# Kernel tuning notes

Hardware: AMD Instinct MI355X
Metric: run time of the kernel (lower is better)

## Reference

```python
import jax, jax.numpy as jnp
import numpy as np

DIM = 1024
HEADS = 16

def setup_inputs() -> dict:
    key = jax.random.key(0)
    ks = jax.random.split(key, 5)
    x = jax.random.normal(ks[0], (4, 2048, DIM), dtype=jnp.float32)
    s = 1.0 / np.sqrt(DIM)
    Wqkv = jax.random.normal(ks[1], (DIM, 3 * DIM), dtype=jnp.float32) * s
    bqkv = jnp.zeros((3 * DIM,), dtype=jnp.float32)
    Wproj = jax.random.normal(ks[2], (DIM, DIM), dtype=jnp.float32) * s
    bproj = jnp.zeros((DIM,), dtype=jnp.float32)
    return {"x": x, "Wqkv": Wqkv, "bqkv": bqkv, "Wproj": Wproj, "bproj": bproj}

def reference(x, Wqkv, bqkv, Wproj, bproj):
    B, N, D = x.shape
    H = HEADS
    hd = D // H
    scale = hd ** (-0.5)
    qkv = x @ Wqkv + bqkv                      # [B, N, 3D]
    q, k, v = jnp.split(qkv, 3, axis=-1)
    # [B, N, H, hd] -> [B, H, N, hd]
    q = q.reshape(B, N, H, hd).transpose(0, 2, 1, 3)
    k = k.reshape(B, N, H, hd).transpose(0, 2, 1, 3)
    v = v.reshape(B, N, H, hd).transpose(0, 2, 1, 3)
    attn = jnp.einsum('bhqd,bhkd->bhqk', q, k) * scale
    attn = jax.nn.softmax(attn, axis=-1)
    out = jnp.einsum('bhqk,bhkd->bhqd', attn, v)
    out = out.transpose(0, 2, 1, 3).reshape(B, N, D)
    return out @ Wproj + bproj
```

## Files before the change

kernel.cpp:

```cpp
#include <hip/hip_runtime.h>
#include <hip/hip_bf16.h>
#include <math.h>


typedef __bf16 bf16;
typedef __bf16 bf16x4 __attribute__((ext_vector_type(4)));
typedef __bf16 bf16x8 __attribute__((ext_vector_type(8)));
typedef float f32x4 __attribute__((ext_vector_type(4)));

#define AS1(p) ((const __attribute__((address_space(1))) void*)(p))
#define AS3(p) ((__attribute__((address_space(3))) void*)(p))

__device__ __forceinline__ void async16(const void* g, void* l) {
    __builtin_amdgcn_global_load_lds(AS1(g), AS3(l), 16, 0, 0);
}

#if __has_builtin(__builtin_amdgcn_exp2f)
#define EXP2(x) __builtin_amdgcn_exp2f(x)
#else
#define EXP2(x) exp2f(x)
#endif

#define QSCALE 0.18033688011112042f


__global__ __launch_bounds__(256) void prep(const float* __restrict__ x,
                                            bf16* __restrict__ xb,
                                            const float* __restrict__ Wqkv,
                                            bf16* __restrict__ wqkvt,
                                            const float* __restrict__ Wproj,
                                            bf16* __restrict__ wprojt) {
    __shared__ float t[32][33];
    const int bx = blockIdx.x;
    const int tid = threadIdx.x;

    if (bx < 8192) {
        const int i = bx * 256 + tid;
        float4 v = ((const float4*)x)[i];
        bf16x4 o;
        o.x = (bf16)v.x; o.y = (bf16)v.y; o.z = (bf16)v.z; o.w = (bf16)v.w;
        ((bf16x4*)xb)[i] = o;
        return;
    }

    const float* in;
    bf16* out;
    int N, n0, k0;
    if (bx < 11264) {
        const int b = bx - 8192;
        in = Wqkv; out = wqkvt; N = 3072;
        n0 = (b % 96) * 32; k0 = (b / 96) * 32;
    } else {
        const int b = bx - 11264;
        in = Wproj; out = wprojt; N = 1024;
        n0 = (b & 31) * 32; k0 = (b >> 5) * 32;
    }
    const int tx = tid & 31, ty = tid >> 5;
    #pragma unroll
    for (int j = 0; j < 32; j += 8)
        t[ty + j][tx] = in[(size_t)(k0 + ty + j) * N + n0 + tx];
    __syncthreads();
    #pragma unroll
    for (int j = 0; j < 32; j += 8)
        out[(size_t)(n0 + ty + j) * 1024 + k0 + tx] = (bf16)t[tx][ty + j];
}


#define GEMM_STAGE(B) do { \
    async16(ga0, la0_##B); async16(ga1, la1_##B); \
    async16(gb0, lb0_##B); async16(gb1, lb1_##B); \
    ga0 += 32; ga1 += 32; gb0 += 32; gb1 += 32; \
} while (0)

#define GEMM_COMPUTE(B) do { \
    bf16x8 af[4], bfr[4]; \
    _Pragma("unroll") \
    for (int i = 0; i < 4; i++) \
        af[i] = *(const bf16x8*)(pa_##B + (wm + i * 16) * 32); \
    _Pragma("unroll") \
    for (int j = 0; j < 4; j++) \
        bfr[j] = *(const bf16x8*)(pb_##B + (wn + j * 16) * 32); \
    _Pragma("unroll") \
    for (int i = 0; i < 4; i++) \
        _Pragma("unroll") \
        for (int j = 0; j < 4; j++) \
            acc[i][j] = __builtin_amdgcn_mfma_f32_16x16x32_bf16(af[i], bfr[j], acc[i][j], 0, 0, 0); \
} while (0)

#define GEMM_SYNC(N) do { \
    asm volatile("s_waitcnt vmcnt(" #N ") lgkmcnt(0)" ::: "memory"); \
    __builtin_amdgcn_s_barrier(); \
    __builtin_amdgcn_sched_barrier(0); \
} while (0)

__device__ __forceinline__ void gemm_mainloop(const bf16* __restrict__ A,
                                              const bf16* __restrict__ Bt,
                                              int K, int m0, int n0,
                                              bf16* As0, bf16* As1, bf16* As2,
                                              bf16* Bs0, bf16* Bs1, bf16* Bs2,
                                              f32x4 acc[4][4]) {
    const int tid = threadIdx.x;
    const int wave = tid >> 6, lane = tid & 63;
    const int c = lane & 15, quad = lane >> 4;
    const int wm = (wave & 1) * 64, wn = (wave >> 1) * 64;

    const int ci0 = (wave * 2 + 0) * 64 + lane;
    const int ci1 = (wave * 2 + 1) * 64 + lane;
    const int cs0 = (ci0 & 3) ^ ((ci0 >> 3) & 3);
    const int cs1 = (ci1 & 3) ^ ((ci1 >> 3) & 3);
    const bf16* ga0 = A  + (size_t)(m0 + (ci0 >> 2)) * K + cs0 * 8;
    const bf16* ga1 = A  + (size_t)(m0 + (ci1 >> 2)) * K + cs1 * 8;
    const bf16* gb0 = Bt + (size_t)(n0 + (ci0 >> 2)) * K + cs0 * 8;
    const bf16* gb1 = Bt + (size_t)(n0 + (ci1 >> 2)) * K + cs1 * 8;
    bf16* la0_0 = As0 + (wave * 2 + 0) * 512;
    bf16* la1_0 = As0 + (wave * 2 + 1) * 512;
    bf16* la0_1 = As1 + (wave * 2 + 0) * 512;
    bf16* la1_1 = As1 + (wave * 2 + 1) * 512;
    bf16* la0_2 = As2 + (wave * 2 + 0) * 512;
    bf16* la1_2 = As2 + (wave * 2 + 1) * 512;
    bf16* lb0_0 = Bs0 + (wave * 2 + 0) * 512;
    bf16* lb1_0 = Bs0 + (wave * 2 + 1) * 512;
    bf16* lb0_1 = Bs1 + (wave * 2 + 0) * 512;
    bf16* lb1_1 = Bs1 + (wave * 2 + 1) * 512;
    bf16* lb0_2 = Bs2 + (wave * 2 + 0) * 512;
    bf16* lb1_2 = Bs2 + (wave * 2 + 1) * 512;

    const int chs = (quad ^ ((c >> 1) & 3)) * 8;
    const bf16* pa_0 = As0 + c * 32 + chs;
    const bf16* pa_1 = As1 + c * 32 + chs;
    const bf16* pa_2 = As2 + c * 32 + chs;
    const bf16* pb_0 = Bs0 + c * 32 + chs;
    const bf16* pb_1 = Bs1 + c * 32 + chs;
    const bf16* pb_2 = Bs2 + c * 32 + chs;

    GEMM_STAGE(0);
    GEMM_STAGE(1);
    for (int t = 0; t < 10; t++) {
        GEMM_SYNC(4); GEMM_STAGE(2); GEMM_COMPUTE(0);
        GEMM_SYNC(4); GEMM_STAGE(0); GEMM_COMPUTE(1);
        GEMM_SYNC(4); GEMM_STAGE(1); GEMM_COMPUTE(2);
    }
    GEMM_SYNC(4); GEMM_COMPUTE(0);
    GEMM_SYNC(0); GEMM_COMPUTE(1);
}


__global__ __launch_bounds__(256, 3) void gemm_qkv(const bf16* __restrict__ A,
                                                   const bf16* __restrict__ Bt,
                                                   const float* __restrict__ bias,
                                                   bf16* __restrict__ Qb,
                                                   bf16* __restrict__ Kb,
                                                   bf16* __restrict__ Vtb) {
    __shared__ __align__(16) bf16 As0[128 * 32];
    __shared__ __align__(16) bf16 As1[128 * 32];
    __shared__ __align__(16) bf16 As2[128 * 32];
    __shared__ __align__(16) bf16 Bs0[128 * 32];
    __shared__ __align__(16) bf16 Bs1[128 * 32];
    __shared__ __align__(16) bf16 Bs2[128 * 32];
    f32x4 acc[4][4] = {};
    const int m0 = blockIdx.x * 128, n0 = blockIdx.y * 128;
    gemm_mainloop(A, Bt, 1024, m0, n0, As0, As1, As2, Bs0, Bs1, Bs2, acc);

    const int tid = threadIdx.x;
    const int wave = tid >> 6, lane = tid & 63;
    const int c = lane & 15, quad = lane >> 4;
    const int wm = (wave & 1) * 64, wn = (wave >> 1) * 64;
    const int sel = n0 >> 10;
    bf16* QK = (sel == 0) ? Qb : Kb;
    const float qs = (sel == 0) ? QSCALE : 1.0f;

    #pragma unroll
    for (int j = 0; j < 4; j++) {
        const int nfull = n0 + wn + j * 16 + c;
        const int nmod = nfull & 1023;
        const int h = nmod >> 6, e = nmod & 63;
        const float bv = bias[nfull];
        #pragma unroll
        for (int i = 0; i < 4; i++) {
            const int mbase = m0 + wm + i * 16 + quad * 4;
            const int b = mbase >> 11, t = mbase & 2047;
            if (sel < 2) {
                bf16* dst = QK + (((size_t)(b * 16 + h) * 2048 + t) * 64 + e);
                #pragma unroll
                for (int r = 0; r < 4; r++)
                    dst[(size_t)r * 64] = (bf16)((acc[i][j][r] + bv) * qs);
            } else {
                bf16* dst = Vtb + ((size_t)(b * 16 + h) * 64 + e) * 2048 + t;
                bf16x4 v;
                v.x = (bf16)(acc[i][j][0] + bv);
                v.y = (bf16)(acc[i][j][1] + bv);
                v.z = (bf16)(acc[i][j][2] + bv);
                v.w = (bf16)(acc[i][j][3] + bv);
                *(bf16x4*)dst = v;
            }
        }
    }
}


#define ATTN_STAGE(B) do { \
    async16(kS0, kD0_##B); async16(kS1, kD1_##B); \
    async16(vS0, vD0_##B); async16(vS1, vD1_##B); \
    kS0 += 4096; kS1 += 4096; vS0 += 64; vS1 += 64; \
} while (0)

#define ATTN_COMPUTE(B) do { \
    _Pragma("unroll") \
    for (int j = 0; j < 4; j++) { \
        bf16x8 kf0 = *(const bf16x8*)(kb0_##B + j * 1024); \
        bf16x8 kf1 = *(const bf16x8*)(kb1_##B + j * 1024); \
        f32x4 s0 = {}, s1 = {}; \
        __builtin_amdgcn_s_setprio(1); \
        s0 = __builtin_amdgcn_mfma_f32_16x16x32_bf16(kf0, qf[0][0], s0, 0, 0, 0); \
        s0 = __builtin_amdgcn_mfma_f32_16x16x32_bf16(kf1, qf[0][1], s0, 0, 0, 0); \
        s1 = __builtin_amdgcn_mfma_f32_16x16x32_bf16(kf0, qf[1][0], s1, 0, 0, 0); \
        s1 = __builtin_amdgcn_mfma_f32_16x16x32_bf16(kf1, qf[1][1], s1, 0, 0, 0); \
        __builtin_amdgcn_s_setprio(0); \
        _Pragma("unroll") \
        for (int r = 0; r < 4; r++) { s0[r] = EXP2(s0[r]); s1[r] = EXP2(s1[r]); } \
        lsum[0] += s0; \
        lsum[1] += s1; \
        bf16x4 p0, p1; \
        p0.x = (bf16)s0[0]; p0.y = (bf16)s0[1]; p0.z = (bf16)s0[2]; p0.w = (bf16)s0[3]; \
        p1.x = (bf16)s1[0]; p1.y = (bf16)s1[1]; p1.z = (bf16)s1[2]; p1.w = (bf16)s1[3]; \
        *(bf16x4*)(pwa + (((j * 4 + quad) ^ sw14) << 2)) = p0; \
        *(bf16x4*)(pwb + (((j * 4 + quad) ^ sw14) << 2)) = p1; \
    } \
    _Pragma("unroll") \
    for (int gks = 0; gks < 2; gks++) { \
        const bf16* vbg = gks ? vb1_##B : vb0_##B; \
        bf16x8 vf[4]; \
        _Pragma("unroll") \
        for (int n2 = 0; n2 < 4; n2++) \
            vf[n2] = *(const bf16x8*)(vbg + n2 * 1024); \
        bf16x8 pf0 = *(const bf16x8*)(pwa + (((gks * 8 + quad * 2) ^ sw14) << 2)); \
        bf16x8 pf1 = *(const bf16x8*)(pwb + (((gks * 8 + quad * 2) ^ sw14) << 2)); \
        __builtin_amdgcn_s_setprio(1); \
        _Pragma("unroll") \
        for (int n2 = 0; n2 < 4; n2++) { \
            o[0][n2] = __builtin_amdgcn_mfma_f32_16x16x32_bf16(pf0, vf[n2], o[0][n2], 0, 0, 0); \
            o[1][n2] = __builtin_amdgcn_mfma_f32_16x16x32_bf16(pf1, vf[n2], o[1][n2], 0, 0, 0); \
        } \
        __builtin_amdgcn_s_setprio(0); \
    } \
} while (0)

__global__ __launch_bounds__(256, 3) void attn_kernel(const bf16* __restrict__ Q,
                                                      const bf16* __restrict__ Kg,
                                                      const bf16* __restrict__ Vt,
                                                      bf16* __restrict__ Out) {
    __shared__ __align__(16) bf16 Ks0[64 * 64];
    __shared__ __align__(16) bf16 Ks1[64 * 64];
    __shared__ __align__(16) bf16 Vs0[64 * 64];
    __shared__ __align__(16) bf16 Vs1[64 * 64];
    __shared__ __align__(16) bf16 Pl[4 * 2 * 16 * 64];

    const int bh = blockIdx.x, qt = blockIdx.y;
    const int tid = threadIdx.x;
    const int wave = tid >> 6, lane = tid & 63;
    const int c = lane & 15, quad = lane >> 4;

    const bf16* Qb = Q + (size_t)bh * 2048 * 64;
    bf16* pw = Pl + wave * 2048;

    const int qbase = qt * 128 + wave * 32;

    bf16x8 qf[2][2];
    #pragma unroll
    for (int i = 0; i < 2; i++)
        #pragma unroll
        for (int ks = 0; ks < 2; ks++)
            qf[i][ks] = *(const bf16x8*)(Qb + (size_t)(qbase + i * 16 + c) * 64 + ks * 32 + quad * 8);

    const int s0i = tid, s1i = 256 + tid;
    const int rk0 = s0i >> 3, cg0 = (s0i & 7) ^ (rk0 & 7);
    const int rk1 = s1i >> 3, cg1 = (s1i & 7) ^ (rk1 & 7);
    const bf16* kS0 = Kg + (size_t)bh * 2048 * 64 + rk0 * 64 + cg0 * 8;
    const bf16* kS1 = Kg + (size_t)bh * 2048 * 64 + rk1 * 64 + cg1 * 8;
    const bf16* vS0 = Vt + (size_t)bh * 64 * 2048 + (size_t)rk0 * 2048 + cg0 * 8;
    const bf16* vS1 = Vt + (size_t)bh * 64 * 2048 + (size_t)rk1 * 2048 + cg1 * 8;
    bf16* kD0_0 = Ks0 + (size_t)(wave * 64) * 8;
    bf16* kD1_0 = Ks0 + (size_t)(256 + wave * 64) * 8;
    bf16* kD0_1 = Ks1 + (size_t)(wave * 64) * 8;
    bf16* kD1_1 = Ks1 + (size_t)(256 + wave * 64) * 8;
    bf16* vD0_0 = Vs0 + (size_t)(wave * 64) * 8;
    bf16* vD1_0 = Vs0 + (size_t)(256 + wave * 64) * 8;
    bf16* vD0_1 = Vs1 + (size_t)(wave * 64) * 8;
    bf16* vD1_1 = Vs1 + (size_t)(256 + wave * 64) * 8;

    const int sw = c & 7;
    const int ch0 = (quad ^ sw) * 8, ch1 = ((quad ^ sw) ^ 4) * 8;
    const bf16* kb0_0 = Ks0 + c * 64 + ch0;
    const bf16* kb1_0 = Ks0 + c * 64 + ch1;
    const bf16* kb0_1 = Ks1 + c * 64 + ch0;
    const bf16* kb1_1 = Ks1 + c * 64 + ch1;
    const bf16* vb0_0 = Vs0 + c * 64 + ch0;
    const bf16* vb1_0 = Vs0 + c * 64 + ch1;
    const bf16* vb0_1 = Vs1 + c * 64 + ch0;
    const bf16* vb1_1 = Vs1 + c * 64 + ch1;
    const int sw14 = c & 14;
    bf16* pwa = pw + c * 64;
    bf16* pwb = pwa + 16 * 64;

    f32x4 lsum[2] = {};
    f32x4 o[2][4] = {};

    ATTN_STAGE(0);
    __syncthreads();
    for (int kv2 = 0; kv2 < 16; kv2++) {
        ATTN_STAGE(1);
        ATTN_COMPUTE(0);
        __syncthreads();
        if (kv2 < 15) ATTN_STAGE(0);
        ATTN_COMPUTE(1);
        __syncthreads();
    }

    const int b = bh >> 4, hh = bh & 15;
    #pragma unroll
    for (int i = 0; i < 2; i++) {
        float lh = (lsum[i][0] + lsum[i][1]) + (lsum[i][2] + lsum[i][3]);
        lh += __shfl_xor(lh, 16);
        lh += __shfl_xor(lh, 32);
        const float li0 = __shfl(lh, quad * 4 + 0);
        const float li1 = __shfl(lh, quad * 4 + 1);
        const float li2 = __shfl(lh, quad * 4 + 2);
        const float li3 = __shfl(lh, quad * 4 + 3);
        const float inv[4] = {1.f / li0, 1.f / li1, 1.f / li2, 1.f / li3};
        #pragma unroll
        for (int r = 0; r < 4; r++) {
            const int token = b * 2048 + qbase + i * 16 + quad * 4 + r;
            #pragma unroll
            for (int n2 = 0; n2 < 4; n2++) {
                const int feat = hh * 64 + n2 * 16 + c;
                Out[(size_t)token * 1024 + feat] = (bf16)(o[i][n2][r] * inv[r]);
            }
        }
    }
}


__global__ __launch_bounds__(256, 3) void gemm_proj(const bf16* __restrict__ A,
                                                    const bf16* __restrict__ Bt,
                                                    const float* __restrict__ bias,
                                                    float* __restrict__ Out) {
    __shared__ __align__(16) bf16 As0[128 * 32];
    __shared__ __align__(16) bf16 As1[128 * 32];
    __shared__ __align__(16) bf16 As2[128 * 32];
    __shared__ __align__(16) bf16 Bs0[128 * 32];
    __shared__ __align__(16) bf16 Bs1[128 * 32];
    __shared__ __align__(16) bf16 Bs2[128 * 32];
    f32x4 acc[4][4] = {};
    const int m0 = blockIdx.x * 128, n0 = blockIdx.y * 128;
    gemm_mainloop(A, Bt, 1024, m0, n0, As0, As1, As2, Bs0, Bs1, Bs2, acc);

    const int tid = threadIdx.x;
    const int wave = tid >> 6, lane = tid & 63;
    const int c = lane & 15, quad = lane >> 4;
    const int wm = (wave & 1) * 64, wn = (wave >> 1) * 64;

    #pragma unroll
    for (int j = 0; j < 4; j++) {
        const int nn = n0 + wn + j * 16 + c;
        const float bv = bias[nn];
        #pragma unroll
        for (int i = 0; i < 4; i++) {
            const int m = m0 + wm + i * 16 + quad * 4;
            #pragma unroll
            for (int r = 0; r < 4; r++)
                Out[(size_t)(m + r) * 1024 + nn] = acc[i][j][r] + bv;
        }
    }
}


extern "C" void kernel_launch(void* const* d_in, const int* in_sizes, int n_in,
                              void* d_out, int out_size, void* d_ws, size_t ws_size,
                              hipStream_t stream) {
    const float* x     = (const float*)d_in[0];
    const float* Wqkv  = (const float*)d_in[1];
    const float* bqkv  = (const float*)d_in[2];
    const float* Wproj = (const float*)d_in[3];
    const float* bproj = (const float*)d_in[4];
    float* out = (float*)d_out;

    char* ws = (char*)d_ws;
    bf16* xb     = (bf16*)(ws);
    bf16* wqkvt  = (bf16*)(ws + 16777216);
    bf16* wprojt = (bf16*)(ws + 23068672);
    bf16* Qb     = (bf16*)(ws + 25165824);
    bf16* Kb     = (bf16*)(ws + 41943040);
    bf16* Vtb    = (bf16*)(ws + 58720256);
    bf16* attno  = xb;

    prep<<<12288, 256, 0, stream>>>(x, xb, Wqkv, wqkvt, Wproj, wprojt);
    gemm_qkv<<<dim3(64, 24), 256, 0, stream>>>(xb, wqkvt, bqkv, Qb, Kb, Vtb);
    attn_kernel<<<dim3(64, 16), 256, 0, stream>>>(Qb, Kb, Vtb, attno);
    gemm_proj<<<dim3(64, 8), 256, 0, stream>>>(attno, wprojt, bproj, out);
}
```

Before: 257.1 us.

## Interleave QK and PV per half-tile to halve P scratch and raise occupancy

Attention compute now alternates between score generation and the P·V product every 32 keys instead of doing all 64 keys of QK^T before P·V. Because of this, each wave's P staging buffer in LDS only has to hold half a tile, which halves it and uses a new rotation-based swizzle. The freed LDS and the launch bound raised from 3 to 4 blocks per CU are meant to increase occupancy and overlap the exp work with MFMA. The risk is register spills under the tighter per-thread budget and bank conflicts from the new swizzle.

New measurement: 273.9 us. 1.07x slower.

```diff
diff --git a/kernel.cpp b/kernel.cpp
--- a/kernel.cpp
+++ b/kernel.cpp
@@ -204,48 +204,50 @@
     kS0 += 4096; kS1 += 4096; vS0 += 64; vS1 += 64; \
 } while (0)
 
+#define ATTN_QKJ(B, j) do { \
+    bf16x8 kf0 = *(const bf16x8*)(kb0_##B + (j) * 1024); \
+    bf16x8 kf1 = *(const bf16x8*)(kb1_##B + (j) * 1024); \
+    f32x4 s0 = {}, s1 = {}; \
+    __builtin_amdgcn_s_setprio(1); \
+    s0 = __builtin_amdgcn_mfma_f32_16x16x32_bf16(kf0, qf[0][0], s0, 0, 0, 0); \
+    s0 = __builtin_amdgcn_mfma_f32_16x16x32_bf16(kf1, qf[0][1], s0, 0, 0, 0); \
+    s1 = __builtin_amdgcn_mfma_f32_16x16x32_bf16(kf0, qf[1][0], s1, 0, 0, 0); \
+    s1 = __builtin_amdgcn_mfma_f32_16x16x32_bf16(kf1, qf[1][1], s1, 0, 0, 0); \
+    __builtin_amdgcn_s_setprio(0); \
+    _Pragma("unroll") \
+    for (int r = 0; r < 4; r++) { s0[r] = EXP2(s0[r]); s1[r] = EXP2(s1[r]); } \
+    lsum[0] += s0; \
+    lsum[1] += s1; \
+    bf16x4 p0, p1; \
+    p0.x = (bf16)s0[0]; p0.y = (bf16)s0[1]; p0.z = (bf16)s0[2]; p0.w = (bf16)s0[3]; \
+    p1.x = (bf16)s1[0]; p1.y = (bf16)s1[1]; p1.z = (bf16)s1[2]; p1.w = (bf16)s1[3]; \
+    *(bf16x4*)(pwa + (((j) & 1) ? pwo1 : pwo0)) = p0; \
+    *(bf16x4*)(pwb + (((j) & 1) ? pwo1 : pwo0)) = p1; \
+} while (0)
+
+#define ATTN_PVG(B, gks) do { \
+    const bf16* vbg = (gks) ? vb1_##B : vb0_##B; \
+    bf16x8 vf[4]; \
+    _Pragma("unroll") \
+    for (int n2 = 0; n2 < 4; n2++) \
+        vf[n2] = *(const bf16x8*)(vbg + n2 * 1024); \
+    bf16x8 pf0 = *(const bf16x8*)(pwa + pro); \
+    bf16x8 pf1 = *(const bf16x8*)(pwb + pro); \
+    __builtin_amdgcn_s_setprio(1); \
+    _Pragma("unroll") \
+    for (int n2 = 0; n2 < 4; n2++) { \
+        o[0][n2] = __builtin_amdgcn_mfma_f32_16x16x32_bf16(pf0, vf[n2], o[0][n2], 0, 0, 0); \
+        o[1][n2] = __builtin_amdgcn_mfma_f32_16x16x32_bf16(pf1, vf[n2], o[1][n2], 0, 0, 0); \
+    } \
+    __builtin_amdgcn_s_setprio(0); \
+} while (0)
+
 #define ATTN_COMPUTE(B) do { \
-    _Pragma("unroll") \
-    for (int j = 0; j < 4; j++) { \
-        bf16x8 kf0 = *(const bf16x8*)(kb0_##B + j * 1024); \
-        bf16x8 kf1 = *(const bf16x8*)(kb1_##B + j * 1024); \
-        f32x4 s0 = {}, s1 = {}; \
-        __builtin_amdgcn_s_setprio(1); \
-        s0 = __builtin_amdgcn_mfma_f32_16x16x32_bf16(kf0, qf[0][0], s0, 0, 0, 0); \
-        s0 = __builtin_amdgcn_mfma_f32_16x16x32_bf16(kf1, qf[0][1], s0, 0, 0, 0); \
-        s1 = __builtin_amdgcn_mfma_f32_16x16x32_bf16(kf0, qf[1][0], s1, 0, 0, 0); \
-        s1 = __builtin_amdgcn_mfma_f32_16x16x32_bf16(kf1, qf[1][1], s1, 0, 0, 0); \
-        __builtin_amdgcn_s_setprio(0); \
-        _Pragma("unroll") \
-        for (int r = 0; r < 4; r++) { s0[r] = EXP2(s0[r]); s1[r] = EXP2(s1[r]); } \
-        lsum[0] += s0; \
-        lsum[1] += s1; \
-        bf16x4 p0, p1; \
-        p0.x = (bf16)s0[0]; p0.y = (bf16)s0[1]; p0.z = (bf16)s0[2]; p0.w = (bf16)s0[3]; \
-        p1.x = (bf16)s1[0]; p1.y = (bf16)s1[1]; p1.z = (bf16)s1[2]; p1.w = (bf16)s1[3]; \
-        *(bf16x4*)(pwa + (((j * 4 + quad) ^ sw14) << 2)) = p0; \
-        *(bf16x4*)(pwb + (((j * 4 + quad) ^ sw14) << 2)) = p1; \
-    } \
-    _Pragma("unroll") \
-    for (int gks = 0; gks < 2; gks++) { \
-        const bf16* vbg = gks ? vb1_##B : vb0_##B; \
-        bf16x8 vf[4]; \
-        _Pragma("unroll") \
-        for (int n2 = 0; n2 < 4; n2++) \
-            vf[n2] = *(const bf16x8*)(vbg + n2 * 1024); \
-        bf16x8 pf0 = *(const bf16x8*)(pwa + (((gks * 8 + quad * 2) ^ sw14) << 2)); \
-        bf16x8 pf1 = *(const bf16x8*)(pwb + (((gks * 8 + quad * 2) ^ sw14) << 2)); \
-        __builtin_amdgcn_s_setprio(1); \
-        _Pragma("unroll") \
-        for (int n2 = 0; n2 < 4; n2++) { \
-            o[0][n2] = __builtin_amdgcn_mfma_f32_16x16x32_bf16(pf0, vf[n2], o[0][n2], 0, 0, 0); \
-            o[1][n2] = __builtin_amdgcn_mfma_f32_16x16x32_bf16(pf1, vf[n2], o[1][n2], 0, 0, 0); \
-        } \
-        __builtin_amdgcn_s_setprio(0); \
-    } \
-} while (0)
-
-__global__ __launch_bounds__(256, 3) void attn_kernel(const bf16* __restrict__ Q,
+    ATTN_QKJ(B, 0); ATTN_QKJ(B, 1); ATTN_PVG(B, 0); \
+    ATTN_QKJ(B, 2); ATTN_QKJ(B, 3); ATTN_PVG(B, 1); \
+} while (0)
+
+__global__ __launch_bounds__(256, 4) void attn_kernel(const bf16* __restrict__ Q,
                                                       const bf16* __restrict__ Kg,
                                                       const bf16* __restrict__ Vt,
                                                       bf16* __restrict__ Out) {
@@ -253,7 +255,7 @@
     __shared__ __align__(16) bf16 Ks1[64 * 64];
     __shared__ __align__(16) bf16 Vs0[64 * 64];
     __shared__ __align__(16) bf16 Vs1[64 * 64];
-    __shared__ __align__(16) bf16 Pl[4 * 2 * 16 * 64];
+    __shared__ __align__(16) bf16 Pl[4 * 1024];
 
     const int bh = blockIdx.x, qt = blockIdx.y;
     const int tid = threadIdx.x;
@@ -261,7 +263,7 @@
     const int c = lane & 15, quad = lane >> 4;
 
     const bf16* Qb = Q + (size_t)bh * 2048 * 64;
-    bf16* pw = Pl + wave * 2048;
+    bf16* pw = Pl + wave * 1024;
 
     const int qbase = qt * 128 + wave * 32;
 
@@ -298,9 +300,13 @@
     const bf16* vb1_0 = Vs0 + c * 64 + ch1;
     const bf16* vb0_1 = Vs1 + c * 64 + ch0;
     const bf16* vb1_1 = Vs1 + c * 64 + ch1;
-    const int sw14 = c & 14;
-    bf16* pwa = pw + c * 64;
-    bf16* pwb = pwa + 16 * 64;
+
+    const int rot = (c >> 1) & 3;
+    bf16* pwa = pw + c * 32;
+    bf16* pwb = pwa + 16 * 32;
+    const int pwo0 = ((((quad >> 1) + rot) & 3) * 8) + (quad & 1) * 4;
+    const int pwo1 = (((2 + (quad >> 1) + rot) & 3) * 8) + (quad & 1) * 4;
+    const int pro  = (((quad + rot) & 3) * 8);
 
     f32x4 lsum[2] = {};
     f32x4 o[2][4] = {};
```
